# Optimization experiments

Measured on AMD Instinct MI355X. Metric: run time of the kernel, lower is better.

## Reference

```python
import jax, jax.numpy as jnp
import numpy as np

TOTAL_COUNT = 500
LN_EPS = 1e-3  # keras LayerNormalization default epsilon
ALPHA_EPS = 1e-6  # keep Dirichlet concentration strictly positive after relu


def setup_inputs() -> dict:
    key = jax.random.key(0)
    k1, k2, k3 = jax.random.split(key, 3)
    C, N, G = 10, 1000, 18000
    return {
        "x": jax.random.normal(k1, (4, 64), dtype=jnp.float32),
        "W": jax.random.normal(k2, (64, 10), dtype=jnp.float32),
        "b": jnp.zeros((10,), dtype=jnp.float32),
        "scdata": jax.random.uniform(k3, (C, N, G), dtype=jnp.float32),
        "gamma": jnp.ones((G,), dtype=jnp.float32),
        "beta": jnp.zeros((G,), dtype=jnp.float32),
    }


def _dirichlet_multinomial_counts(key, alpha, total_count):
    # alpha: [B, K] -> counts [B, K] summing to total_count per row
    kg, kc = jax.random.split(key)
    g = jax.random.gamma(kg, alpha)                      # [B, K] Dirichlet via Gamma
    p = g / jnp.sum(g, axis=-1, keepdims=True)
    logits = jnp.log(p)
    draws = jax.random.categorical(kc, logits, shape=(total_count,) + alpha.shape[:1])  # [T, B]
    counts = jnp.sum(jax.nn.one_hot(draws, alpha.shape[-1], dtype=jnp.int32), axis=0)   # [B, K]
    return counts


def reference(x, W, b, scdata, gamma, beta):
    key = jax.random.key(42)
    k_dir, k_sub = jax.random.split(key)

    # Dense(10, relu)
    alpha = jax.nn.relu(x @ W + b) + ALPHA_EPS           # [B, 10]
    counts = _dirichlet_multinomial_counts(k_dir, alpha, TOTAL_COUNT)  # [B, 10]
    counts0 = counts[0]                                  # only first batch row used

    # Per-celltype: shuffle rows, take first k_c, sum -> equivalent to a random
    # without-replacement row subset. Expressed as a masked matvec (no gather).
    C, N, G = scdata.shape
    keys = jax.random.split(k_sub, C)

    def subsample_weights(key_c, k_c):
        perm = jax.random.permutation(key_c, N)
        mask = (jnp.arange(N) < k_c).astype(scdata.dtype)
        return jnp.zeros((N,), dtype=scdata.dtype).at[perm].set(mask)

    w = jax.vmap(subsample_weights)(keys, counts0)       # [C, N]
    total = jnp.einsum("cn,cng->g", w, scdata)           # Add over celltypes fused in

    # log1p -> LayerNorm(last axis) -> MinMax
    z = jnp.log1p(total)
    mean = jnp.mean(z)
    var = jnp.mean(jnp.square(z - mean))
    z = (z - mean) * jax.lax.rsqrt(var + LN_EPS) * gamma + beta
    lo, hi = jnp.min(z), jnp.max(z)
    denom = hi - lo
    return jnp.where(denom == 0, jnp.zeros_like(z), (z - lo) / jnp.where(denom == 0, 1.0, denom))
```

## Files before the change

### kernel.cpp

```cpp
#include <hip/hip_runtime.h>
#include <stdint.h>

#pragma clang fp contract(off)

#define JAX_PARTITIONABLE 1

struct KeyT { uint32_t a, b; };

__device__ __forceinline__ void tf_round(uint32_t &x0, uint32_t &x1, int r) {
  x0 += x1;
  x1 = (x1 << r) | (x1 >> (32 - r));
  x1 ^= x0;
}

__device__ KeyT tf(KeyT k, uint32_t x0, uint32_t x1) {
  uint32_t ks2 = k.a ^ k.b ^ 0x1BD11BDAu;
  x0 += k.a; x1 += k.b;
  tf_round(x0, x1, 13); tf_round(x0, x1, 15); tf_round(x0, x1, 26); tf_round(x0, x1, 6);
  x0 += k.b; x1 += ks2 + 1u;
  tf_round(x0, x1, 17); tf_round(x0, x1, 29); tf_round(x0, x1, 16); tf_round(x0, x1, 24);
  x0 += ks2; x1 += k.a + 2u;
  tf_round(x0, x1, 13); tf_round(x0, x1, 15); tf_round(x0, x1, 26); tf_round(x0, x1, 6);
  x0 += k.a; x1 += k.b + 3u;
  tf_round(x0, x1, 17); tf_round(x0, x1, 29); tf_round(x0, x1, 16); tf_round(x0, x1, 24);
  x0 += k.b; x1 += ks2 + 4u;
  tf_round(x0, x1, 13); tf_round(x0, x1, 15); tf_round(x0, x1, 26); tf_round(x0, x1, 6);
  x0 += ks2; x1 += k.a + 5u;
  KeyT o; o.a = x0; o.b = x1;
  return o;
}

__device__ uint32_t rb32(KeyT key, uint32_t size, uint32_t i) {
#if JAX_PARTITIONABLE
  (void)size;
  KeyT o = tf(key, 0u, i);
  return o.a ^ o.b;
#else
  uint32_t h = (size + 1u) >> 1;
  if (i < h) {
    uint32_t partner = h + i;
    if (partner >= size) partner = 0u;
    return tf(key, i, partner).a;
  } else {
    return tf(key, i - h, i).b;
  }
#endif
}

__device__ KeyT key_split(KeyT key, uint32_t n, uint32_t j) {
#if JAX_PARTITIONABLE
  (void)n;
  return tf(key, 0u, j);
#else
  KeyT r;
  uint32_t i0 = 2u * j, i1 = 2u * j + 1u;
  r.a = (i0 < n) ? tf(key, i0, i0 + n).a : tf(key, i0 - n, i0).b;
  r.b = (i1 < n) ? tf(key, i1, i1 + n).a : tf(key, i1 - n, i1).b;
  return r;
#endif
}

__device__ __forceinline__ float u01_from_bits(uint32_t bits) {
  return __uint_as_float((bits >> 9) | 0x3f800000u) - 1.0f;
}

__device__ float erfinv_xla(float x) {
  float w = -log1pf(-x * x);
  float p;
  if (w < 5.0f) {
    w = w - 2.5f;
    p = 2.81022636e-08f;
    p = 3.43273939e-07f + p * w;
    p = -3.5233877e-06f + p * w;
    p = -4.39150654e-06f + p * w;
    p = 0.00021858087f + p * w;
    p = -0.00125372503f + p * w;
    p = -0.00417768164f + p * w;
    p = 0.246640727f + p * w;
    p = 1.50140941f + p * w;
  } else {
    w = sqrtf(w) - 3.0f;
    p = -0.000200214257f;
    p = 0.000100950558f + p * w;
    p = 0.00134934322f + p * w;
    p = -0.00367342844f + p * w;
    p = 0.00573950773f + p * w;
    p = -0.0076224613f + p * w;
    p = 0.00943887047f + p * w;
    p = 1.00167406f + p * w;
    p = 2.83297682f + p * w;
  }
  return p * x;
}

__device__ float uniform01_scalar(KeyT key) {
  return u01_from_bits(rb32(key, 1u, 0u));
}

__device__ float normal_scalar(KeyT key) {
  uint32_t bits = rb32(key, 1u, 0u);
  float f = u01_from_bits(bits);
  const float lo = -0.99999994f;
  float u = f * 2.0f + lo;
  u = fmaxf(lo, u);
  return 1.41421354f * erfinv_xla(u);
}

__device__ float gamma_one(KeyT key, float alpha) {
  KeyT sub = key_split(key, 2u, 1u);
  KeyT nk  = key_split(key, 2u, 0u);
  key = nk;
  bool boost_mask = (alpha >= 1.0f);
  float alpha_eff = boost_mask ? alpha : (alpha + 1.0f);
  float d = alpha_eff - 0.33333334f;
  float c = 0.33333334f / sqrtf(d);
  float X = 0.0f, V = 1.0f, U = 2.0f;
  while ((U >= 1.0f - 0.0331f * (X * X)) &&
         (logf(U) >= 0.5f * X + d - d * V + d * logf(V))) {
    KeyT k0 = key_split(key, 3u, 0u);
    KeyT xk = key_split(key, 3u, 1u);
    KeyT Uk = key_split(key, 3u, 2u);
    key = k0;
    float x = 0.0f, v = -1.0f;
    KeyT ik = xk;
    while (v <= 0.0f) {
      KeyT ik2 = key_split(ik, 2u, 0u);
      KeyT sk  = key_split(ik, 2u, 1u);
      ik = ik2;
      x = normal_scalar(sk);
      v = 1.0f + c * x;
    }
    X = x * x;
    V = (v * v) * v;
    U = uniform01_scalar(Uk);
  }
  float s = d * V;
  if (!boost_mask) {
    s = s * powf(uniform01_scalar(sub), 1.0f / alpha);
  }
  return s;
}

#define GDIM 18000
#define NROW 1000
#define NCT  10
#define TCNT 500

__global__ __launch_bounds__(256) void bs_rng(const float* __restrict__ x,
                                              const float* __restrict__ W,
                                              const float* __restrict__ bias,
                                              int* __restrict__ counts,
                                              float* __restrict__ totals) {
  int tid = threadIdx.x;
  for (int g = tid; g < GDIM; g += 256) totals[g] = 0.0f;

  __shared__ float gs[NCT];
  __shared__ float lg[NCT];
  __shared__ int   cnt[NCT];
  if (tid < NCT) cnt[tid] = 0;

  KeyT root;  root.a = 0u; root.b = 42u;
  KeyT k_dir = key_split(root, 2u, 0u);
  KeyT kg    = key_split(k_dir, 2u, 0u);
  KeyT kc    = key_split(k_dir, 2u, 1u);

  if (tid < NCT) {
    int k = tid;
    float acc = 0.0f;
    for (int i = 0; i < 64; ++i) acc += x[i] * W[i * NCT + k];
    acc += bias[k];
    float alpha = fmaxf(acc, 0.0f) + 1e-6f;
    KeyT gk = key_split(kg, 40u, (uint32_t)k);
    gs[k] = gamma_one(gk, alpha);
  }
  __syncthreads();
  if (tid == 0) {
    float s = 0.0f;
    for (int k = 0; k < NCT; ++k) s += gs[k];
    for (int k = 0; k < NCT; ++k) lg[k] = logf(gs[k] / s);
  }
  __syncthreads();

  const float tiny = 1.17549435e-38f;
  for (int t = tid; t < TCNT; t += 256) {
    float best = -__builtin_inff();
    int bi = 0;
#pragma unroll
    for (int k = 0; k < NCT; ++k) {
      uint32_t idx = (uint32_t)(t * 40 + k);
      uint32_t bits = rb32(kc, 20000u, idx);
      float f = u01_from_bits(bits);
      float u = fmaxf(tiny, f + tiny);
      float gum = -logf(-logf(u));
      float val = gum + lg[k];
      if (val > best) { best = val; bi = k; }
    }
    atomicAdd(&cnt[bi], 1);
  }
  __syncthreads();
  if (tid < NCT) counts[tid] = cnt[tid];
}

__global__ __launch_bounds__(256) void bs_perm(const int* __restrict__ counts,
                                               int* __restrict__ rows) {
  int c = blockIdx.x;
  int tid = threadIdx.x;
  __shared__ uint32_t sb[NROW];
  __shared__ int kc_s, pre_s, slot;
  if (tid == 0) {
    slot = 0;
    int pre = 0;
    for (int i = 0; i < c; ++i) pre += counts[i];
    pre_s = pre;
    kc_s = counts[c];
  }
  KeyT root;  root.a = 0u; root.b = 42u;
  KeyT k_sub = key_split(root, 2u, 1u);
  KeyT ck    = key_split(k_sub, (uint32_t)NCT, (uint32_t)c);
  KeyT sk    = key_split(ck, 2u, 1u);
  for (int n = tid; n < NROW; n += 256) sb[n] = rb32(sk, (uint32_t)NROW, (uint32_t)n);
  __syncthreads();

  const int n0 = tid, n1 = tid + 256, n2 = tid + 512, n3 = tid + 768;
  const bool has3 = (n3 < NROW);
  uint32_t b0 = sb[n0], b1 = sb[n1], b2 = sb[n2];
  uint32_t b3 = has3 ? sb[n3] : 0u;
  int r0 = 0, r1 = 0, r2 = 0, r3 = 0;

  const uint4* sb4 = (const uint4*)sb;
#pragma unroll 5
  for (int q = 0; q < NROW / 4; ++q) {
    uint4 v = sb4[q];
    int m = q * 4;
#define RANK_STEP(BM, MM)                                              \
    r0 += (BM < b0) || (BM == b0 && (MM) < n0);                        \
    r1 += (BM < b1) || (BM == b1 && (MM) < n1);                        \
    r2 += (BM < b2) || (BM == b2 && (MM) < n2);                        \
    r3 += (BM < b3) || (BM == b3 && (MM) < n3);
    RANK_STEP(v.x, m)
    RANK_STEP(v.y, m + 1)
    RANK_STEP(v.z, m + 2)
    RANK_STEP(v.w, m + 3)
#undef RANK_STEP
  }

  int kc = kc_s, pre = pre_s;
  if (r0 < kc)          rows[pre + atomicAdd(&slot, 1)] = c * NROW + n0;
  if (r1 < kc)          rows[pre + atomicAdd(&slot, 1)] = c * NROW + n1;
  if (r2 < kc)          rows[pre + atomicAdd(&slot, 1)] = c * NROW + n2;
  if (has3 && r3 < kc)  rows[pre + atomicAdd(&slot, 1)] = c * NROW + n3;
}

__global__ __launch_bounds__(256) void bs_sum(const float* __restrict__ sc,
                                              const int* __restrict__ rows,
                                              float* __restrict__ totals) {
  __shared__ int rloc[25];
  int tid = threadIdx.x;
  int base = blockIdx.y * 25;
  if (tid < 25) rloc[tid] = rows[base + tid];
  __syncthreads();
  int g = blockIdx.x * 256 + tid;
  if (g < GDIM) {
    float acc = 0.0f;
#pragma unroll
    for (int i = 0; i < 25; ++i) {
      long long off = (long long)rloc[i] * GDIM + g;
      acc += sc[off];
    }
    atomicAdd(&totals[g], acc);
  }
}

#define NPT 18
__global__ __launch_bounds__(1024) void bs_norm(float* __restrict__ totals,
                                                const float* __restrict__ gma,
                                                const float* __restrict__ bta,
                                                float* __restrict__ out) {
  int tid = threadIdx.x;
  __shared__ double red[1024];
  float z[NPT];
  double s = 0.0;
#pragma unroll
  for (int j = 0; j < NPT; ++j) {
    int g = tid + j * 1024;
    float zz = (g < GDIM) ? log1pf(totals[g]) : 0.0f;
    z[j] = zz;
    s += (double)zz;
  }
  red[tid] = s; __syncthreads();
  for (int st = 512; st > 0; st >>= 1) { if (tid < st) red[tid] += red[tid + st]; __syncthreads(); }
  float mean = (float)(red[0] / (double)GDIM);
  __syncthreads();

  double v = 0.0;
#pragma unroll
  for (int j = 0; j < NPT; ++j) {
    int g = tid + j * 1024;
    if (g < GDIM) { float d = z[j] - mean; v += (double)d * (double)d; }
  }
  red[tid] = v; __syncthreads();
  for (int st = 512; st > 0; st >>= 1) { if (tid < st) red[tid] += red[tid + st]; __syncthreads(); }
  float var = (float)(red[0] / (double)GDIM);
  __syncthreads();

  float rs = rsqrtf(var + 1e-3f);
  float mn = 3.4e38f, mx = -3.4e38f;
#pragma unroll
  for (int j = 0; j < NPT; ++j) {
    int g = tid + j * 1024;
    if (g < GDIM) {
      float zn = (z[j] - mean) * rs * gma[g] + bta[g];
      z[j] = zn;
      mn = fminf(mn, zn);
      mx = fmaxf(mx, zn);
    }
  }
  red[tid] = (double)mn; __syncthreads();
  for (int st = 512; st > 0; st >>= 1) { if (tid < st) red[tid] = fmin(red[tid], red[tid + st]); __syncthreads(); }
  float lo = (float)red[0]; __syncthreads();
  red[tid] = (double)mx; __syncthreads();
  for (int st = 512; st > 0; st >>= 1) { if (tid < st) red[tid] = fmax(red[tid], red[tid + st]); __syncthreads(); }
  float hi = (float)red[0];
  float denom = hi - lo;
#pragma unroll
  for (int j = 0; j < NPT; ++j) {
    int g = tid + j * 1024;
    if (g < GDIM) out[g] = (denom == 0.0f) ? 0.0f : (z[j] - lo) / denom;
  }
}

extern "C" void kernel_launch(void* const* d_in, const int* in_sizes, int n_in,
                              void* d_out, int out_size, void* d_ws, size_t ws_size,
                              hipStream_t stream) {
  (void)in_sizes; (void)n_in; (void)out_size; (void)ws_size;
  const float* x   = (const float*)d_in[0];
  const float* W   = (const float*)d_in[1];
  const float* b   = (const float*)d_in[2];
  const float* sc  = (const float*)d_in[3];
  const float* gma = (const float*)d_in[4];
  const float* bta = (const float*)d_in[5];
  float* out = (float*)d_out;

  int* counts = (int*)d_ws;
  int* rows   = counts + 16;
  float* totals = out;

  hipLaunchKernelGGL(bs_rng,  dim3(1),      dim3(256),  0, stream, x, W, b, counts, totals);
  hipLaunchKernelGGL(bs_perm, dim3(10),     dim3(256),  0, stream, counts, rows);
  hipLaunchKernelGGL(bs_sum,  dim3(71, 20), dim3(256),  0, stream, sc, rows, totals);
  hipLaunchKernelGGL(bs_norm, dim3(1),      dim3(1024), 0, stream, totals, gma, bta, out);
}
```

Measured before the change: 895.2 us.

## Split permutation ranking across blocks, vectorize row sum, use wave-shuffle reductions

The permutation-ranking kernel now runs as 4x10 blocks, each thread ranking one row, with per-celltype slot counters moved to global memory and zeroed in the RNG kernel. The gather-sum kernel loads float4 per thread, so it needs four times fewer threads and blocks. The normalization kernel replaces shared-memory tree reductions with wavefront shuffle reductions. Together these aim to cut serial latency in the small kernels and memory instruction count in the sum, at the cost of more global atomics.

```diff
diff --git a/kernel.cpp b/kernel.cpp
--- a/kernel.cpp
+++ b/kernel.cpp
@@ -150,9 +150,11 @@
                                               const float* __restrict__ W,
                                               const float* __restrict__ bias,
                                               int* __restrict__ counts,
+                                              int* __restrict__ slots,
                                               float* __restrict__ totals) {
   int tid = threadIdx.x;
   for (int g = tid; g < GDIM; g += 256) totals[g] = 0.0f;
+  if (tid < NCT) slots[tid] = 0;
 
   __shared__ float gs[NCT];
   __shared__ float lg[NCT];
@@ -202,13 +204,13 @@
 }
 
 __global__ __launch_bounds__(256) void bs_perm(const int* __restrict__ counts,
+                                               int* __restrict__ slots,
                                                int* __restrict__ rows) {
-  int c = blockIdx.x;
+  int c = blockIdx.y;
   int tid = threadIdx.x;
   __shared__ uint32_t sb[NROW];
-  __shared__ int kc_s, pre_s, slot;
+  __shared__ int kc_s, pre_s;
   if (tid == 0) {
-    slot = 0;
     int pre = 0;
     for (int i = 0; i < c; ++i) pre += counts[i];
     pre_s = pre;
@@ -221,34 +223,24 @@
   for (int n = tid; n < NROW; n += 256) sb[n] = rb32(sk, (uint32_t)NROW, (uint32_t)n);
   __syncthreads();
 
-  const int n0 = tid, n1 = tid + 256, n2 = tid + 512, n3 = tid + 768;
-  const bool has3 = (n3 < NROW);
-  uint32_t b0 = sb[n0], b1 = sb[n1], b2 = sb[n2];
-  uint32_t b3 = has3 ? sb[n3] : 0u;
-  int r0 = 0, r1 = 0, r2 = 0, r3 = 0;
-
+  const int  n0  = blockIdx.x * 250 + tid;
+  const bool act = (tid < 250);
+  uint32_t b0 = act ? sb[n0] : 0u;
+  int r0 = 0;
   const uint4* sb4 = (const uint4*)sb;
 #pragma unroll 5
   for (int q = 0; q < NROW / 4; ++q) {
     uint4 v = sb4[q];
     int m = q * 4;
-#define RANK_STEP(BM, MM)                                              \
-    r0 += (BM < b0) || (BM == b0 && (MM) < n0);                        \
-    r1 += (BM < b1) || (BM == b1 && (MM) < n1);                        \
-    r2 += (BM < b2) || (BM == b2 && (MM) < n2);                        \
-    r3 += (BM < b3) || (BM == b3 && (MM) < n3);
-    RANK_STEP(v.x, m)
-    RANK_STEP(v.y, m + 1)
-    RANK_STEP(v.z, m + 2)
-    RANK_STEP(v.w, m + 3)
-#undef RANK_STEP
-  }
-
-  int kc = kc_s, pre = pre_s;
-  if (r0 < kc)          rows[pre + atomicAdd(&slot, 1)] = c * NROW + n0;
-  if (r1 < kc)          rows[pre + atomicAdd(&slot, 1)] = c * NROW + n1;
-  if (r2 < kc)          rows[pre + atomicAdd(&slot, 1)] = c * NROW + n2;
-  if (has3 && r3 < kc)  rows[pre + atomicAdd(&slot, 1)] = c * NROW + n3;
+    r0 += (v.x < b0) || (v.x == b0 && m     < n0);
+    r0 += (v.y < b0) || (v.y == b0 && m + 1 < n0);
+    r0 += (v.z < b0) || (v.z == b0 && m + 2 < n0);
+    r0 += (v.w < b0) || (v.w == b0 && m + 3 < n0);
+  }
+  if (act && r0 < kc_s) {
+    int s = atomicAdd(&slots[c], 1);
+    rows[pre_s + s] = c * NROW + n0;
+  }
 }
 
 __global__ __launch_bounds__(256) void bs_sum(const float* __restrict__ sc,
@@ -259,16 +251,79 @@
   int base = blockIdx.y * 25;
   if (tid < 25) rloc[tid] = rows[base + tid];
   __syncthreads();
-  int g = blockIdx.x * 256 + tid;
-  if (g < GDIM) {
-    float acc = 0.0f;
+  int e4 = blockIdx.x * 256 + tid;
+  if (e4 < GDIM / 4) {
+    int g = e4 * 4;
+    float ax = 0.0f, ay = 0.0f, az = 0.0f, aw = 0.0f;
 #pragma unroll
     for (int i = 0; i < 25; ++i) {
-      long long off = (long long)rloc[i] * GDIM + g;
-      acc += sc[off];
+      const float4 v = *(const float4*)(sc + (size_t)rloc[i] * GDIM + g);
+      ax += v.x; ay += v.y; az += v.z; aw += v.w;
     }
-    atomicAdd(&totals[g], acc);
-  }
+    atomicAdd(&totals[g],     ax);
+    atomicAdd(&totals[g + 1], ay);
+    atomicAdd(&totals[g + 2], az);
+    atomicAdd(&totals[g + 3], aw);
+  }
+}
+
+__device__ __forceinline__ double wred_add(double v) {
+#pragma unroll
+  for (int o = 32; o > 0; o >>= 1) v += __shfl_down(v, o, 64);
+  return v;
+}
+__device__ __forceinline__ float wred_min(float v) {
+#pragma unroll
+  for (int o = 32; o > 0; o >>= 1) v = fminf(v, __shfl_down(v, o, 64));
+  return v;
+}
+__device__ __forceinline__ float wred_max(float v) {
+#pragma unroll
+  for (int o = 32; o > 0; o >>= 1) v = fmaxf(v, __shfl_down(v, o, 64));
+  return v;
+}
+
+__device__ double block_add(double v, double* wbuf, int tid) {
+  int lane = tid & 63, wid = tid >> 6;
+  double t = wred_add(v);
+  __syncthreads();
+  if (lane == 0) wbuf[wid] = t;
+  __syncthreads();
+  if (wid == 0) {
+    double x = (lane < 16) ? wbuf[lane] : 0.0;
+    x = wred_add(x);
+    if (lane == 0) wbuf[16] = x;
+  }
+  __syncthreads();
+  return wbuf[16];
+}
+__device__ float block_min(float v, double* wbuf, int tid) {
+  int lane = tid & 63, wid = tid >> 6;
+  float t = wred_min(v);
+  __syncthreads();
+  if (lane == 0) wbuf[wid] = (double)t;
+  __syncthreads();
+  if (wid == 0) {
+    float x = (lane < 16) ? (float)wbuf[lane] : 3.4e38f;
+    x = wred_min(x);
+    if (lane == 0) wbuf[16] = (double)x;
+  }
+  __syncthreads();
+  return (float)wbuf[16];
+}
+__device__ float block_max(float v, double* wbuf, int tid) {
+  int lane = tid & 63, wid = tid >> 6;
+  float t = wred_max(v);
+  __syncthreads();
+  if (lane == 0) wbuf[wid] = (double)t;
+  __syncthreads();
+  if (wid == 0) {
+    float x = (lane < 16) ? (float)wbuf[lane] : -3.4e38f;
+    x = wred_max(x);
+    if (lane == 0) wbuf[16] = (double)x;
+  }
+  __syncthreads();
+  return (float)wbuf[16];
 }
 
 #define NPT 18
@@ -277,7 +332,7 @@
                                                 const float* __restrict__ bta,
                                                 float* __restrict__ out) {
   int tid = threadIdx.x;
-  __shared__ double red[1024];
+  __shared__ double wbuf[17];
   float z[NPT];
   double s = 0.0;
 #pragma unroll
@@ -287,10 +342,7 @@
     z[j] = zz;
     s += (double)zz;
   }
-  red[tid] = s; __syncthreads();
-  for (int st = 512; st > 0; st >>= 1) { if (tid < st) red[tid] += red[tid + st]; __syncthreads(); }
-  float mean = (float)(red[0] / (double)GDIM);
-  __syncthreads();
+  float mean = (float)(block_add(s, wbuf, tid) / (double)GDIM);
 
   double v = 0.0;
 #pragma unroll
@@ -298,10 +350,7 @@
     int g = tid + j * 1024;
     if (g < GDIM) { float d = z[j] - mean; v += (double)d * (double)d; }
   }
-  red[tid] = v; __syncthreads();
-  for (int st = 512; st > 0; st >>= 1) { if (tid < st) red[tid] += red[tid + st]; __syncthreads(); }
-  float var = (float)(red[0] / (double)GDIM);
-  __syncthreads();
+  float var = (float)(block_add(v, wbuf, tid) / (double)GDIM);
 
   float rs = rsqrtf(var + 1e-3f);
   float mn = 3.4e38f, mx = -3.4e38f;
@@ -315,12 +364,8 @@
       mx = fmaxf(mx, zn);
     }
   }
-  red[tid] = (double)mn; __syncthreads();
-  for (int st = 512; st > 0; st >>= 1) { if (tid < st) red[tid] = fmin(red[tid], red[tid + st]); __syncthreads(); }
-  float lo = (float)red[0]; __syncthreads();
-  red[tid] = (double)mx; __syncthreads();
-  for (int st = 512; st > 0; st >>= 1) { if (tid < st) red[tid] = fmax(red[tid], red[tid + st]); __syncthreads(); }
-  float hi = (float)red[0];
+  float lo = block_min(mn, wbuf, tid);
+  float hi = block_max(mx, wbuf, tid);
   float denom = hi - lo;
 #pragma unroll
   for (int j = 0; j < NPT; ++j) {
@@ -342,11 +387,12 @@
   float* out = (float*)d_out;
 
   int* counts = (int*)d_ws;
-  int* rows   = counts + 16;
+  int* slots  = counts + 16;
+  int* rows   = counts + 32;
   float* totals = out;
 
-  hipLaunchKernelGGL(bs_rng,  dim3(1),      dim3(256),  0, stream, x, W, b, counts, totals);
-  hipLaunchKernelGGL(bs_perm, dim3(10),     dim3(256),  0, stream, counts, rows);
-  hipLaunchKernelGGL(bs_sum,  dim3(71, 20), dim3(256),  0, stream, sc, rows, totals);
+  hipLaunchKernelGGL(bs_rng,  dim3(1),      dim3(256),  0, stream, x, W, b, counts, slots, totals);
+  hipLaunchKernelGGL(bs_perm, dim3(4, 10),  dim3(256),  0, stream, counts, slots, rows);
+  hipLaunchKernelGGL(bs_sum,  dim3(18, 20), dim3(256),  0, stream, sc, rows, totals);
   hipLaunchKernelGGL(bs_norm, dim3(1),      dim3(1024), 0, stream, totals, gma, bta, out);
 }
```

Result: faster. 835.3 us (-6.7%).
